# Kernel tuning notes

Hardware: AMD Instinct MI355X
Metric: run time of the kernel (lower is better)

Reference implementation:

```python
import jax, jax.numpy as jnp
import numpy as np

B, N, DIM = 4, 2048, 1024
HEADS, DIM_HEAD = 16, 64
INNER = HEADS * DIM_HEAD  # 1024
SCALE = DIM_HEAD ** -0.5

def setup_inputs() -> dict:
    key = jax.random.key(0)
    k1, k2, k3 = jax.random.split(key, 3)
    x = jax.random.normal(k1, (B, N, DIM), dtype=jnp.float32)
    w_qkv = jax.random.normal(k2, (DIM, 3 * INNER), dtype=jnp.float32) * (DIM ** -0.5)
    w_out = jax.random.normal(k3, (INNER, DIM), dtype=jnp.float32) * (INNER ** -0.5)
    b_out = jnp.zeros((DIM,), dtype=jnp.float32)
    return {"x": x, "w_qkv": w_qkv, "w_out": w_out, "b_out": b_out}

def reference(x, w_qkv, w_out, b_out):
    b, n, _ = x.shape
    qkv = x @ w_qkv  # [b, n, 3*inner]
    q, k, v = jnp.split(qkv, 3, axis=-1)
    # [b, n, h, d] -> [b, h, n, d]
    reshape = lambda t: t.reshape(b, n, HEADS, DIM_HEAD).transpose(0, 2, 1, 3)
    q, k, v = reshape(q), reshape(k), reshape(v)
    dots = jnp.einsum('bhqd,bhkd->bhqk', q, k) * SCALE
    attn = jax.nn.softmax(dots, axis=-1)
    out = jnp.einsum('bhqk,bhkd->bhqd', attn, v)
    out = out.transpose(0, 2, 1, 3).reshape(b, n, INNER)
    return out @ w_out + b_out
```

## Files before the change

### kernel.cpp

```cpp
#include <hip/hip_runtime.h>

typedef unsigned short u16;
typedef __bf16 bf16_t;
typedef bf16_t bf16x8 __attribute__((ext_vector_type(8)));
typedef float f32x4 __attribute__((ext_vector_type(4)));
typedef u16 u16x8 __attribute__((ext_vector_type(8)));
typedef u16 u16x4 __attribute__((ext_vector_type(4)));

#define B_     4
#define N_     2048
#define DIM_   1024
#define HEADS_ 16
#define DH_    64
#define INNER_ 1024
#define QKV3_  3072
#define SCALE_ 0.125f

__device__ __forceinline__ u16 f2bf(float f) {
  union { float f; unsigned u; } v; v.f = f;
  unsigned r = v.u + 0x7FFFu + ((v.u >> 16) & 1u);
  return (u16)(r >> 16);
}
__device__ __forceinline__ u16 bfbits(float f) {
  bf16_t b = (bf16_t)f;
  return __builtin_bit_cast(u16, b);
}

__global__ __launch_bounds__(256) void cvt_f32_bf16(const float* __restrict__ in,
                                                    u16* __restrict__ out, int n8) {
  int i = blockIdx.x * 256 + threadIdx.x;
  if (i < n8) {
    const float4* p = (const float4*)(in + (size_t)i * 8);
    float4 a = p[0], b = p[1];
    u16x8 o;
    o[0] = f2bf(a.x); o[1] = f2bf(a.y); o[2] = f2bf(a.z); o[3] = f2bf(a.w);
    o[4] = f2bf(b.x); o[5] = f2bf(b.y); o[6] = f2bf(b.z); o[7] = f2bf(b.w);
    *(u16x8*)(out + (size_t)i * 8) = o;
  }
}

__global__ __launch_bounds__(256) void transp_w(const float* __restrict__ in,
                                                u16* __restrict__ out, int Kd, int Nd) {
  __shared__ float t[32][33];
  int n0 = blockIdx.x * 32, k0 = blockIdx.y * 32;
  int tx = threadIdx.x & 31, ty = threadIdx.x >> 5;
#pragma unroll
  for (int i = 0; i < 4; i++)
    t[ty + i * 8][tx] = in[(size_t)(k0 + ty + i * 8) * Nd + n0 + tx];
  __syncthreads();
#pragma unroll
  for (int i = 0; i < 4; i++)
    out[(size_t)(n0 + ty + i * 8) * Kd + k0 + tx] = f2bf(t[tx][ty + i * 8]);
}

__global__ __launch_bounds__(256) void transp_v(const u16* __restrict__ qkv,
                                                u16* __restrict__ vT) {
  __shared__ u16 t[32][33];
  int bh = blockIdx.z; int b = bh >> 4, h = bh & 15;
  int n0 = blockIdx.x * 32, d0 = blockIdx.y * 32;
  int tx = threadIdx.x & 31, ty = threadIdx.x >> 5;
#pragma unroll
  for (int i = 0; i < 4; i++)
    t[ty + i * 8][tx] =
        qkv[(size_t)(b * N_ + n0 + ty + i * 8) * QKV3_ + 2 * INNER_ + h * DH_ + d0 + tx];
  __syncthreads();
#pragma unroll
  for (int i = 0; i < 4; i++)
    vT[((size_t)bh * DH_ + d0 + ty + i * 8) * N_ + n0 + tx] = t[tx][ty + i * 8];
}

template <int F32OUT>
__global__ __launch_bounds__(256) void gemm_bt(const u16* __restrict__ A,
                                               const u16* __restrict__ BT,
                                               void* __restrict__ Cp,
                                               const float* __restrict__ bias,
                                               int M, int N, int K) {
  __shared__ alignas(16) u16 ldsA[128 * 64];
  __shared__ alignas(16) u16 ldsB[128 * 64];
  const int tid = threadIdx.x;
  const int lane = tid & 63, wid = tid >> 6;
  const int l16 = lane & 15, lg = lane >> 4;
  const int ntiles = N >> 7;
  const int tm = blockIdx.x / ntiles, tn = blockIdx.x % ntiles;
  const int m0 = tm << 7, n0 = tn << 7;
  const int wr = wid >> 1, wc = wid & 1;

  f32x4 acc[4][4];
#pragma unroll
  for (int i = 0; i < 4; i++)
#pragma unroll
    for (int j = 0; j < 4; j++) acc[i][j] = f32x4{0.f, 0.f, 0.f, 0.f};

  for (int k0 = 0; k0 < K; k0 += 64) {
#pragma unroll
    for (int i = 0; i < 4; i++) {
      int c = i * 256 + tid;
      int row = c >> 3, slot = c & 7;
      uint4 va = *(const uint4*)(A  + (size_t)(m0 + row) * K + k0 + slot * 8);
      uint4 vb = *(const uint4*)(BT + (size_t)(n0 + row) * K + k0 + slot * 8);
      int off = row * 128 + ((slot * 16) ^ ((row & 7) << 4));
      *(uint4*)((char*)ldsA + off) = va;
      *(uint4*)((char*)ldsB + off) = vb;
    }
    __syncthreads();

    bf16x8 bf[4][2];
#pragma unroll
    for (int n = 0; n < 4; n++) {
      int row = wc * 64 + n * 16 + l16;
      int rb = row * 128, swz = (row & 7) << 4;
      bf[n][0] = *(const bf16x8*)((char*)ldsB + rb + ((lg * 16) ^ swz));
      bf[n][1] = *(const bf16x8*)((char*)ldsB + rb + ((64 + lg * 16) ^ swz));
    }
#pragma unroll
    for (int mm = 0; mm < 4; mm++) {
      int row = wr * 64 + mm * 16 + l16;
      int rb = row * 128, swz = (row & 7) << 4;
      bf16x8 af0 = *(const bf16x8*)((char*)ldsA + rb + ((lg * 16) ^ swz));
      bf16x8 af1 = *(const bf16x8*)((char*)ldsA + rb + ((64 + lg * 16) ^ swz));
#pragma unroll
      for (int n = 0; n < 4; n++) {
        acc[mm][n] = __builtin_amdgcn_mfma_f32_16x16x32_bf16(af0, bf[n][0], acc[mm][n], 0, 0, 0);
        acc[mm][n] = __builtin_amdgcn_mfma_f32_16x16x32_bf16(af1, bf[n][1], acc[mm][n], 0, 0, 0);
      }
    }
    __syncthreads();
  }

#pragma unroll
  for (int mm = 0; mm < 4; mm++) {
#pragma unroll
    for (int n = 0; n < 4; n++) {
      int row = m0 + wr * 64 + mm * 16 + lg * 4;
      int col = n0 + wc * 64 + n * 16 + l16;
#pragma unroll
      for (int j = 0; j < 4; j++) {
        if (F32OUT)
          ((float*)Cp)[(size_t)(row + j) * N + col] = acc[mm][n][j] + bias[col];
        else
          ((u16*)Cp)[(size_t)(row + j) * N + col] = f2bf(acc[mm][n][j]);
      }
    }
  }
}

__global__ __launch_bounds__(256) void attn_fwd(const u16* __restrict__ qkv,
                                                const u16* __restrict__ vT,
                                                u16* __restrict__ abuf) {
  __shared__ alignas(16) u16 ldsK[2][64 * 64];
  __shared__ alignas(16) u16 ldsV[2][64 * 64];
  __shared__ alignas(16) u16 plds[4][32 * 64];

  const int tid = threadIdx.x;
  const int lane = tid & 63, wid = tid >> 6;
  const int l16 = lane & 15, lg = lane >> 4;

  int bid = blockIdx.x;
  bid = (bid & 7) * 128 + (bid >> 3);
  const int bh = bid >> 4, qt = bid & 15;
  const int b = bh >> 4, h = bh & 15;
  const int q0 = qt * 128 + wid * 32;

  bf16x8 qf[2][2];
#pragma unroll
  for (int mm = 0; mm < 2; mm++) {
    const u16* qrow = qkv + (size_t)(b * N_ + q0 + mm * 16 + l16) * QKV3_ + h * DH_;
    bf16x8 t0 = *(const bf16x8*)(qrow + lg * 8);
    bf16x8 t1 = *(const bf16x8*)(qrow + 32 + lg * 8);
#pragma unroll
    for (int i = 0; i < 8; i++) {
      t0[i] = (bf16_t)((float)t0[i] * SCALE_);
      t1[i] = (bf16_t)((float)t1[i] * SCALE_);
    }
    qf[mm][0] = t0; qf[mm][1] = t1;
  }

  const int srow = tid >> 3, sslot = tid & 7;
  const u16* ksrc = qkv + (size_t)(b * N_ + srow) * QKV3_ + INNER_ + h * DH_ + sslot * 8;
  const u16* vsrc = vT + ((size_t)bh * DH_ + srow) * N_ + sslot * 8;
  const int wo0 = srow * 128 + ((sslot * 16) ^ ((srow & 7) << 4));
  const int wo1 = wo0 + 32 * 128;

  char* pwave = (char*)&plds[wid][0];

  float mrow[2], lrow[2];
  f32x4 acc[2][4];
#pragma unroll
  for (int mm = 0; mm < 2; mm++) { mrow[mm] = -1e30f; lrow[mm] = 0.f; }
#pragma unroll
  for (int mm = 0; mm < 2; mm++)
#pragma unroll
    for (int d = 0; d < 4; d++) acc[mm][d] = f32x4{0.f, 0.f, 0.f, 0.f};

  {
    uint4 k0 = *(const uint4*)(ksrc);
    uint4 k1 = *(const uint4*)(ksrc + (size_t)32 * QKV3_);
    uint4 v0 = *(const uint4*)(vsrc);
    uint4 v1 = *(const uint4*)(vsrc + 32 * N_);
    *(uint4*)((char*)&ldsK[0][0] + wo0) = k0;
    *(uint4*)((char*)&ldsK[0][0] + wo1) = k1;
    *(uint4*)((char*)&ldsV[0][0] + wo0) = v0;
    *(uint4*)((char*)&ldsV[0][0] + wo1) = v1;
  }

  const int NT = N_ / 64;
  for (int kt = 0; kt < NT; ++kt) {
    const int cur = kt & 1;
    uint4 kr0, kr1, vr0, vr1;
    if (kt < NT - 1) {
      const u16* kp = ksrc + (size_t)(kt + 1) * 64 * QKV3_;
      const u16* vp = vsrc + (kt + 1) * 64;
      kr0 = *(const uint4*)(kp);
      kr1 = *(const uint4*)(kp + (size_t)32 * QKV3_);
      vr0 = *(const uint4*)(vp);
      vr1 = *(const uint4*)(vp + 32 * N_);
    }
    __syncthreads();

    const char* Kb = (const char*)&ldsK[cur][0];
    const char* Vb = (const char*)&ldsV[cur][0];

    f32x4 s[2][4];
#pragma unroll
    for (int kc = 0; kc < 4; kc++) {
      int r = kc * 16 + l16;
      const char* rb = Kb + r * 128;
      int swz = (r & 7) << 4;
      bf16x8 kf0 = *(const bf16x8*)(rb + ((lg * 16) ^ swz));
      bf16x8 kf1 = *(const bf16x8*)(rb + ((64 + lg * 16) ^ swz));
#pragma unroll
      for (int mm = 0; mm < 2; mm++) {
        f32x4 c = f32x4{0.f, 0.f, 0.f, 0.f};
        c = __builtin_amdgcn_mfma_f32_16x16x32_bf16(kf0, qf[mm][0], c, 0, 0, 0);
        c = __builtin_amdgcn_mfma_f32_16x16x32_bf16(kf1, qf[mm][1], c, 0, 0, 0);
        s[mm][kc] = c;
      }
    }

#pragma unroll
    for (int mm = 0; mm < 2; mm++) {
      f32x4 mv0, mv1;
#pragma unroll
      for (int j = 0; j < 4; j++) {
        mv0[j] = fmaxf(s[mm][0][j], s[mm][1][j]);
        mv1[j] = fmaxf(s[mm][2][j], s[mm][3][j]);
      }
      float t = fmaxf(fmaxf(fmaxf(mv0[0], mv0[1]), fmaxf(mv0[2], mv0[3])),
                      fmaxf(fmaxf(mv1[0], mv1[1]), fmaxf(mv1[2], mv1[3])));
      t = fmaxf(t, __shfl_xor(t, 16));
      t = fmaxf(t, __shfl_xor(t, 32));
      float mn = fmaxf(mrow[mm], t);
      if (__ballot(mn - mrow[mm] > 8.f)) {
        float alpha = __expf(mrow[mm] - mn);
        mrow[mm] = mn;
        lrow[mm] *= alpha;
#pragma unroll
        for (int dd = 0; dd < 4; dd++)
#pragma unroll
          for (int j = 0; j < 4; j++) acc[mm][dd][j] *= alpha;
      }
      float psum = 0.f;
      int r = mm * 16 + l16;
      int swz = (r & 7) << 4;
#pragma unroll
      for (int kc = 0; kc < 4; kc++) {
        float p0 = __expf(s[mm][kc][0] - mrow[mm]);
        float p1 = __expf(s[mm][kc][1] - mrow[mm]);
        float p2 = __expf(s[mm][kc][2] - mrow[mm]);
        float p3 = __expf(s[mm][kc][3] - mrow[mm]);
        psum += (p0 + p1) + (p2 + p3);
        u16x4 w;
        w[0] = bfbits(p0); w[1] = bfbits(p1); w[2] = bfbits(p2); w[3] = bfbits(p3);
        *(u16x4*)(pwave + r * 128 + ((kc * 32 + lg * 8) ^ swz)) = w;
      }
      psum += __shfl_xor(psum, 16);
      psum += __shfl_xor(psum, 32);
      lrow[mm] += psum;
    }

    bf16x8 pa[2][2];
#pragma unroll
    for (int mm = 0; mm < 2; mm++) {
      int r = mm * 16 + l16;
      int swz = (r & 7) << 4;
#pragma unroll
      for (int ks = 0; ks < 2; ks++)
        pa[mm][ks] = *(const bf16x8*)(pwave + r * 128 + ((ks * 64 + lg * 16) ^ swz));
    }
#pragma unroll
    for (int dd = 0; dd < 4; dd++) {
      int r = dd * 16 + l16;
      const char* rb = Vb + r * 128;
      int swz = (r & 7) << 4;
      bf16x8 vf0 = *(const bf16x8*)(rb + ((lg * 16) ^ swz));
      bf16x8 vf1 = *(const bf16x8*)(rb + ((64 + lg * 16) ^ swz));
#pragma unroll
      for (int mm = 0; mm < 2; mm++) {
        acc[mm][dd] = __builtin_amdgcn_mfma_f32_16x16x32_bf16(vf0, pa[mm][0], acc[mm][dd], 0, 0, 0);
        acc[mm][dd] = __builtin_amdgcn_mfma_f32_16x16x32_bf16(vf1, pa[mm][1], acc[mm][dd], 0, 0, 0);
      }
    }

    if (kt < NT - 1) {
      char* Kn = (char*)&ldsK[cur ^ 1][0];
      char* Vn = (char*)&ldsV[cur ^ 1][0];
      *(uint4*)(Kn + wo0) = kr0;
      *(uint4*)(Kn + wo1) = kr1;
      *(uint4*)(Vn + wo0) = vr0;
      *(uint4*)(Vn + wo1) = vr1;
    }
  }

#pragma unroll
  for (int mm = 0; mm < 2; mm++) {
    float inv = 1.f / lrow[mm];
    size_t row = (size_t)(b * N_ + q0 + mm * 16 + l16);
#pragma unroll
    for (int dd = 0; dd < 4; dd++) {
      u16x4 w;
#pragma unroll
      for (int j = 0; j < 4; j++) w[j] = bfbits(acc[mm][dd][j] * inv);
      *(u16x4*)(abuf + row * INNER_ + h * DH_ + dd * 16 + lg * 4) = w;
    }
  }
}

extern "C" void kernel_launch(void* const* d_in, const int* in_sizes, int n_in,
                              void* d_out, int out_size, void* d_ws, size_t ws_size,
                              hipStream_t stream) {
  const float* x     = (const float*)d_in[0];
  const float* w_qkv = (const float*)d_in[1];
  const float* w_out = (const float*)d_in[2];
  const float* b_out = (const float*)d_in[3];
  float* out = (float*)d_out;

  char* ws = (char*)d_ws;
  u16* xb    = (u16*)(ws);
  u16* wqkvT = (u16*)(ws + (size_t)(16 << 20));
  u16* woutT = (u16*)(ws + (size_t)(22 << 20));
  u16* qkv   = (u16*)(ws + (size_t)(24 << 20));
  u16* vTb   = (u16*)(ws + (size_t)(72 << 20));
  u16* abuf  = xb;

  cvt_f32_bf16<<<4096, 256, 0, stream>>>(x, xb, (B_ * N_ * DIM_) / 8);
  transp_w<<<dim3(QKV3_ / 32, DIM_ / 32), 256, 0, stream>>>(w_qkv, wqkvT, DIM_, QKV3_);
  transp_w<<<dim3(DIM_ / 32, INNER_ / 32), 256, 0, stream>>>(w_out, woutT, INNER_, DIM_);
  gemm_bt<0><<<(B_ * N_ / 128) * (QKV3_ / 128), 256, 0, stream>>>(
      xb, wqkvT, qkv, nullptr, B_ * N_, QKV3_, DIM_);
  transp_v<<<dim3(N_ / 32, DH_ / 32, B_ * HEADS_), 256, 0, stream>>>(qkv, vTb);
  attn_fwd<<<1024, 256, 0, stream>>>(qkv, vTb, abuf);
  gemm_bt<1><<<(B_ * N_ / 128) * (DIM_ / 128), 256, 0, stream>>>(
      abuf, woutT, out, b_out, B_ * N_, DIM_, INNER_);
}
```

Before: 232.6 us.

## Use direct global-to-LDS loads in GEMM and attention, enlarge attention blocks

Both the GEMM and attention kernels now copy their tiles with global_load_lds, which writes global memory straight into LDS instead of staging through registers. The XOR swizzle moves to the source address, so the existing swizzled LDS reads still work. The attention kernel now runs 512-thread blocks of 8 waves sharing each K/V tile, which halves redundant K/V traffic. It also uses exp2 with a folded log2e FMA and raises wave priority around the MFMA sections. The risks are an unverified LDS ordering at the loop barrier and higher LDS use per block from the larger P buffer.

```diff
diff --git a/kernel.cpp b/kernel.cpp
--- a/kernel.cpp
+++ b/kernel.cpp
@@ -15,6 +15,7 @@
 #define INNER_ 1024
 #define QKV3_  3072
 #define SCALE_ 0.125f
+#define LOG2E_ 1.44269504089f
 
 __device__ __forceinline__ u16 f2bf(float f) {
   union { float f; unsigned u; } v; v.f = f;
@@ -24,6 +25,18 @@
 __device__ __forceinline__ u16 bfbits(float f) {
   bf16_t b = (bf16_t)f;
   return __builtin_bit_cast(u16, b);
+}
+
+#if __has_builtin(__builtin_amdgcn_exp2f)
+#define EXP2F(x) __builtin_amdgcn_exp2f(x)
+#else
+#define EXP2F(x) __expf((x) * 0.69314718056f)
+#endif
+
+typedef __attribute__((address_space(1))) const unsigned int ga_u32;
+typedef __attribute__((address_space(3))) unsigned int ls_u32;
+__device__ __forceinline__ void gload16(const void* g, void* l) {
+  __builtin_amdgcn_global_load_lds((ga_u32*)g, (ls_u32*)l, 16, 0, 0);
 }
 
 __global__ __launch_bounds__(256) void cvt_f32_bf16(const float* __restrict__ in,
@@ -85,6 +98,9 @@
   const int m0 = tm << 7, n0 = tn << 7;
   const int wr = wid >> 1, wc = wid & 1;
 
+  const int srow_in = lane >> 3;
+  const int soff = ((lane & 7) ^ srow_in) * 8;
+
   f32x4 acc[4][4];
 #pragma unroll
   for (int i = 0; i < 4; i++)
@@ -94,13 +110,11 @@
   for (int k0 = 0; k0 < K; k0 += 64) {
 #pragma unroll
     for (int i = 0; i < 4; i++) {
-      int c = i * 256 + tid;
-      int row = c >> 3, slot = c & 7;
-      uint4 va = *(const uint4*)(A  + (size_t)(m0 + row) * K + k0 + slot * 8);
-      uint4 vb = *(const uint4*)(BT + (size_t)(n0 + row) * K + k0 + slot * 8);
-      int off = row * 128 + ((slot * 16) ^ ((row & 7) << 4));
-      *(uint4*)((char*)ldsA + off) = va;
-      *(uint4*)((char*)ldsB + off) = vb;
+      const int rbase = wid * 32 + i * 8;
+      gload16(A  + (size_t)(m0 + rbase + srow_in) * K + k0 + soff,
+              (char*)ldsA + rbase * 128);
+      gload16(BT + (size_t)(n0 + rbase + srow_in) * K + k0 + soff,
+              (char*)ldsB + rbase * 128);
     }
     __syncthreads();
 
@@ -144,22 +158,22 @@
   }
 }
 
-__global__ __launch_bounds__(256) void attn_fwd(const u16* __restrict__ qkv,
-                                                const u16* __restrict__ vT,
-                                                u16* __restrict__ abuf) {
+__global__ __launch_bounds__(512, 4) void attn_fwd(const u16* __restrict__ qkv,
+                                                   const u16* __restrict__ vT,
+                                                   u16* __restrict__ abuf) {
   __shared__ alignas(16) u16 ldsK[2][64 * 64];
   __shared__ alignas(16) u16 ldsV[2][64 * 64];
-  __shared__ alignas(16) u16 plds[4][32 * 64];
+  __shared__ alignas(16) u16 plds[8][32 * 64];
 
   const int tid = threadIdx.x;
   const int lane = tid & 63, wid = tid >> 6;
   const int l16 = lane & 15, lg = lane >> 4;
 
   int bid = blockIdx.x;
-  bid = (bid & 7) * 128 + (bid >> 3);
-  const int bh = bid >> 4, qt = bid & 15;
+  bid = (bid & 7) * 64 + (bid >> 3);
+  const int bh = bid >> 3, qt = bid & 7;
   const int b = bh >> 4, h = bh & 15;
-  const int q0 = qt * 128 + wid * 32;
+  const int q0 = qt * 256 + wid * 32;
 
   bf16x8 qf[2][2];
 #pragma unroll
@@ -175,11 +189,11 @@
     qf[mm][0] = t0; qf[mm][1] = t1;
   }
 
-  const int srow = tid >> 3, sslot = tid & 7;
-  const u16* ksrc = qkv + (size_t)(b * N_ + srow) * QKV3_ + INNER_ + h * DH_ + sslot * 8;
-  const u16* vsrc = vT + ((size_t)bh * DH_ + srow) * N_ + sslot * 8;
-  const int wo0 = srow * 128 + ((sslot * 16) ^ ((srow & 7) << 4));
-  const int wo1 = wo0 + 32 * 128;
+  const int srow = (wid << 3) + (lane >> 3);
+  const int sswz = (lane & 7) ^ (srow & 7);
+  const u16* ksrc = qkv + (size_t)(b * N_ + srow) * QKV3_ + INNER_ + h * DH_ + sswz * 8;
+  const u16* vsrc = vT + ((size_t)bh * DH_ + srow) * N_ + sswz * 8;
+  const int sdst = wid << 10;
 
   char* pwave = (char*)&plds[wid][0];
 
@@ -192,35 +206,23 @@
 #pragma unroll
     for (int d = 0; d < 4; d++) acc[mm][d] = f32x4{0.f, 0.f, 0.f, 0.f};
 
-  {
-    uint4 k0 = *(const uint4*)(ksrc);
-    uint4 k1 = *(const uint4*)(ksrc + (size_t)32 * QKV3_);
-    uint4 v0 = *(const uint4*)(vsrc);
-    uint4 v1 = *(const uint4*)(vsrc + 32 * N_);
-    *(uint4*)((char*)&ldsK[0][0] + wo0) = k0;
-    *(uint4*)((char*)&ldsK[0][0] + wo1) = k1;
-    *(uint4*)((char*)&ldsV[0][0] + wo0) = v0;
-    *(uint4*)((char*)&ldsV[0][0] + wo1) = v1;
-  }
+  gload16(ksrc, (char*)&ldsK[0][0] + sdst);
+  gload16(vsrc, (char*)&ldsV[0][0] + sdst);
+  __syncthreads();
 
   const int NT = N_ / 64;
   for (int kt = 0; kt < NT; ++kt) {
     const int cur = kt & 1;
-    uint4 kr0, kr1, vr0, vr1;
     if (kt < NT - 1) {
-      const u16* kp = ksrc + (size_t)(kt + 1) * 64 * QKV3_;
-      const u16* vp = vsrc + (kt + 1) * 64;
-      kr0 = *(const uint4*)(kp);
-      kr1 = *(const uint4*)(kp + (size_t)32 * QKV3_);
-      vr0 = *(const uint4*)(vp);
-      vr1 = *(const uint4*)(vp + 32 * N_);
-    }
-    __syncthreads();
+      gload16(ksrc + (size_t)(kt + 1) * 64 * QKV3_, (char*)&ldsK[cur ^ 1][0] + sdst);
+      gload16(vsrc + (kt + 1) * 64, (char*)&ldsV[cur ^ 1][0] + sdst);
+    }
 
     const char* Kb = (const char*)&ldsK[cur][0];
     const char* Vb = (const char*)&ldsV[cur][0];
 
     f32x4 s[2][4];
+    __builtin_amdgcn_s_setprio(1);
 #pragma unroll
     for (int kc = 0; kc < 4; kc++) {
       int r = kc * 16 + l16;
@@ -236,17 +238,15 @@
         s[mm][kc] = c;
       }
     }
+    __builtin_amdgcn_s_setprio(0);
 
 #pragma unroll
     for (int mm = 0; mm < 2; mm++) {
-      f32x4 mv0, mv1;
-#pragma unroll
-      for (int j = 0; j < 4; j++) {
-        mv0[j] = fmaxf(s[mm][0][j], s[mm][1][j]);
-        mv1[j] = fmaxf(s[mm][2][j], s[mm][3][j]);
-      }
-      float t = fmaxf(fmaxf(fmaxf(mv0[0], mv0[1]), fmaxf(mv0[2], mv0[3])),
-                      fmaxf(fmaxf(mv1[0], mv1[1]), fmaxf(mv1[2], mv1[3])));
+      float t = fmaxf(fmaxf(fmaxf(s[mm][0][0], s[mm][0][1]), fmaxf(s[mm][0][2], s[mm][0][3])),
+                      fmaxf(fmaxf(s[mm][1][0], s[mm][1][1]), fmaxf(s[mm][1][2], s[mm][1][3])));
+      float u = fmaxf(fmaxf(fmaxf(s[mm][2][0], s[mm][2][1]), fmaxf(s[mm][2][2], s[mm][2][3])),
+                      fmaxf(fmaxf(s[mm][3][0], s[mm][3][1]), fmaxf(s[mm][3][2], s[mm][3][3])));
+      t = fmaxf(t, u);
       t = fmaxf(t, __shfl_xor(t, 16));
       t = fmaxf(t, __shfl_xor(t, 32));
       float mn = fmaxf(mrow[mm], t);
@@ -259,15 +259,16 @@
 #pragma unroll
           for (int j = 0; j < 4; j++) acc[mm][dd][j] *= alpha;
       }
+      const float nm2 = -mrow[mm] * LOG2E_;
       float psum = 0.f;
       int r = mm * 16 + l16;
       int swz = (r & 7) << 4;
 #pragma unroll
       for (int kc = 0; kc < 4; kc++) {
-        float p0 = __expf(s[mm][kc][0] - mrow[mm]);
-        float p1 = __expf(s[mm][kc][1] - mrow[mm]);
-        float p2 = __expf(s[mm][kc][2] - mrow[mm]);
-        float p3 = __expf(s[mm][kc][3] - mrow[mm]);
+        float p0 = EXP2F(__builtin_fmaf(s[mm][kc][0], LOG2E_, nm2));
+        float p1 = EXP2F(__builtin_fmaf(s[mm][kc][1], LOG2E_, nm2));
+        float p2 = EXP2F(__builtin_fmaf(s[mm][kc][2], LOG2E_, nm2));
+        float p3 = EXP2F(__builtin_fmaf(s[mm][kc][3], LOG2E_, nm2));
         psum += (p0 + p1) + (p2 + p3);
         u16x4 w;
         w[0] = bfbits(p0); w[1] = bfbits(p1); w[2] = bfbits(p2); w[3] = bfbits(p3);
@@ -287,6 +288,7 @@
       for (int ks = 0; ks < 2; ks++)
         pa[mm][ks] = *(const bf16x8*)(pwave + r * 128 + ((ks * 64 + lg * 16) ^ swz));
     }
+    __builtin_amdgcn_s_setprio(1);
 #pragma unroll
     for (int dd = 0; dd < 4; dd++) {
       int r = dd * 16 + l16;
@@ -300,15 +302,9 @@
         acc[mm][dd] = __builtin_amdgcn_mfma_f32_16x16x32_bf16(vf1, pa[mm][1], acc[mm][dd], 0, 0, 0);
       }
     }
-
-    if (kt < NT - 1) {
-      char* Kn = (char*)&ldsK[cur ^ 1][0];
-      char* Vn = (char*)&ldsV[cur ^ 1][0];
-      *(uint4*)(Kn + wo0) = kr0;
-      *(uint4*)(Kn + wo1) = kr1;
-      *(uint4*)(Vn + wo0) = vr0;
-      *(uint4*)(Vn + wo1) = vr1;
-    }
+    __builtin_amdgcn_s_setprio(0);
+
+    __syncthreads();
   }
 
 #pragma unroll
@@ -348,7 +344,7 @@
   gemm_bt<0><<<(B_ * N_ / 128) * (QKV3_ / 128), 256, 0, stream>>>(
       xb, wqkvT, qkv, nullptr, B_ * N_, QKV3_, DIM_);
   transp_v<<<dim3(N_ / 32, DH_ / 32, B_ * HEADS_), 256, 0, stream>>>(qkv, vTb);
-  attn_fwd<<<1024, 256, 0, stream>>>(qkv, vTb, abuf);
+  attn_fwd<<<512, 512, 0, stream>>>(qkv, vTb, abuf);
   gemm_bt<1><<<(B_ * N_ / 128) * (DIM_ / 128), 256, 0, stream>>>(
       abuf, woutT, out, b_out, B_ * N_, DIM_, INNER_);
 }
```

Result: faster. 210.8 us (-9.4%).
